# Kernel tuning notes

Measured on AMD Instinct MI355X. Metric: run time of the kernel, lower is better.

## Reference

```python
import jax, jax.numpy as jnp
import numpy as np

N_USERS = 50000
N_PRODS = 50000
N_NODES = N_USERS + N_PRODS
N_EDGES = 600000
UD, PD, H, O = 64, 100, 128, 16


def _gcn_conv(x, W, b, src, dst, n):
    """PyG GCNConv: linear transform, add self-loops, sym-normalized scatter-add."""
    x = x @ W                                    # [n, H]
    loop = jnp.arange(n, dtype=src.dtype)
    src = jnp.concatenate([src, loop])
    dst = jnp.concatenate([dst, loop])
    deg = jax.ops.segment_sum(jnp.ones_like(dst, dtype=x.dtype), dst, num_segments=n)
    dinv = jnp.where(deg > 0, jax.lax.rsqrt(deg), 0.0)
    norm = dinv[src] * dinv[dst]                 # [E+n]
    msg = x[src] * norm[:, None]                 # gather + scale
    out = jax.ops.segment_sum(msg, dst, num_segments=n)
    return out + b


def setup_inputs() -> dict:
    key = jax.random.key(0)
    ks = jax.random.split(key, 16)
    s = 0.05
    return {
        "user_feats": jax.random.normal(ks[0], (N_USERS, UD), dtype=jnp.float32),
        "prod_feats": jax.random.normal(ks[1], (N_PRODS, PD), dtype=jnp.float32),
        "edge_index": jax.random.randint(ks[2], (2, N_EDGES), 0, N_NODES, dtype=jnp.int64),
        "Wu": jax.random.normal(ks[3], (UD, H), dtype=jnp.float32) * s,
        "bu": jnp.zeros((H,), dtype=jnp.float32),
        "Wp": jax.random.normal(ks[4], (PD, H), dtype=jnp.float32) * s,
        "bp": jnp.zeros((H,), dtype=jnp.float32),
        "W1": jax.random.normal(ks[5], (H, H), dtype=jnp.float32) * s,
        "b1": jnp.zeros((H,), dtype=jnp.float32),
        "W2": jax.random.normal(ks[6], (H, H), dtype=jnp.float32) * s,
        "b2": jnp.zeros((H,), dtype=jnp.float32),
        "W3": jax.random.normal(ks[7], (H, H), dtype=jnp.float32) * s,
        "b3": jnp.zeros((H,), dtype=jnp.float32),
        "Wo": jax.random.normal(ks[8], (H, O), dtype=jnp.float32) * s,
        "bo": jnp.zeros((O,), dtype=jnp.float32),
    }


def reference(user_feats, prod_feats, edge_index, Wu, bu, Wp, bp,
              W1, b1, W2, b2, W3, b3, Wo, bo):
    src, dst = edge_index[0], edge_index[1]
    user_x = user_feats @ Wu + bu
    prod_x = prod_feats @ Wp + bp
    x = jnp.concatenate([user_x, prod_x], axis=0)   # [N_NODES, H]
    x = jax.nn.relu(_gcn_conv(x, W1, b1, src, dst, N_NODES))
    # dropout p=0.6 is identity in eval mode
    x = jax.nn.relu(_gcn_conv(x, W2, b2, src, dst, N_NODES))
    x = jax.nn.relu(_gcn_conv(x, W3, b3, src, dst, N_NODES))
    return x @ Wo + bo                              # [N_NODES, O]
```

## Files before the change

kernel.cpp:

```cpp
#include <hip/hip_runtime.h>
#include <hip/hip_fp16.h>

#define NU 50000
#define NP 50000
#define NN 100000
#define NE 600000
#define H  128
#define O  16

typedef __attribute__((ext_vector_type(8))) _Float16 half8;
typedef __attribute__((ext_vector_type(4))) _Float16 h4v;
typedef __attribute__((ext_vector_type(4))) float f32x4;

__global__ void k_prep(const float* __restrict__ Wu, const float* __restrict__ Wp,
                       const float* __restrict__ W1, const float* __restrict__ W2,
                       const float* __restrict__ W3, const float* __restrict__ Wo,
                       __half* __restrict__ whU, __half* __restrict__ wlU,
                       __half* __restrict__ whP, __half* __restrict__ wlP,
                       __half* __restrict__ wh1, __half* __restrict__ wl1,
                       __half* __restrict__ wh2, __half* __restrict__ wl2,
                       __half* __restrict__ wh3, __half* __restrict__ wl3,
                       __half* __restrict__ whO, __half* __restrict__ wlO,
                       int* __restrict__ cnt, int2* __restrict__ epack) {
    int idx = blockIdx.x * blockDim.x + threadIdx.x;
    if (idx >= 75776) {
        int i = idx - 75776;
        if (i < NN) cnt[i] = 0;
        else if (i < NN + 8) { int2 z; z.x = 0; z.y = 0; epack[NE + (i - NN)] = z; }
        return;
    }
    const float* W; __half *Wh, *Wl; int K, KPAD, NC;
    if      (idx <  8192) {              W = Wu; Wh = whU; Wl = wlU; K =  64; KPAD =  64; NC = 128; }
    else if (idx < 24576) { idx -=  8192; W = Wp; Wh = whP; Wl = wlP; K = 100; KPAD = 128; NC = 128; }
    else if (idx < 40960) { idx -= 24576; W = W1; Wh = wh1; Wl = wl1; K = 128; KPAD = 128; NC = 128; }
    else if (idx < 57344) { idx -= 40960; W = W2; Wh = wh2; Wl = wl2; K = 128; KPAD = 128; NC = 128; }
    else if (idx < 73728) { idx -= 57344; W = W3; Wh = wh3; Wl = wl3; K = 128; KPAD = 128; NC = 128; }
    else                  { idx -= 73728; W = Wo; Wh = whO; Wl = wlO; K = 128; KPAD = 128; NC =  16; }
    int n = idx / KPAD, k = idx - n * KPAD;
    float x = (k < K) ? W[k * NC + n] * 16.0f : 0.0f;
    __half h = __float2half_rn(x);
    __half l = __float2half_rn(x - __half2float(h));
    Wh[idx] = h; Wl[idx] = l;
}

__global__ void k_count(const int* __restrict__ dst, int* __restrict__ cnt,
                        int* __restrict__ rank, int E) {
    int e = blockIdx.x * blockDim.x + threadIdx.x;
    if (e < E) rank[e] = atomicAdd(&cnt[dst[e]], 1);
}

#define SCAN_TPB 256
#define SCAN_VPT 4
#define SCAN_CHUNK (SCAN_TPB * SCAN_VPT)

__global__ void k_scan1(const int* __restrict__ in, int* __restrict__ out,
                        int* __restrict__ bsums, float* __restrict__ dinv, int n) {
    __shared__ int sh[SCAN_TPB];
    int t = threadIdx.x, b = blockIdx.x;
    int base = b * SCAN_CHUNK + t * SCAN_VPT;
    int v[SCAN_VPT]; int s = 0;
#pragma unroll
    for (int i = 0; i < SCAN_VPT; i++) {
        int idx = base + i;
        v[i] = (idx < n) ? in[idx] : 0;
        if (idx < n) dinv[idx] = rsqrtf((float)(v[i] + 1));
        s += v[i];
    }
    sh[t] = s; __syncthreads();
    for (int off = 1; off < SCAN_TPB; off <<= 1) {
        int x = (t >= off) ? sh[t - off] : 0;
        __syncthreads();
        sh[t] += x;
        __syncthreads();
    }
    int run = (t > 0) ? sh[t - 1] : 0;
    if (t == SCAN_TPB - 1) bsums[b] = sh[t];
#pragma unroll
    for (int i = 0; i < SCAN_VPT; i++) {
        int idx = base + i;
        if (idx < n) out[idx] = run;
        run += v[i];
    }
}

__global__ void k_scan2(int* __restrict__ bsums, int nb) {
    __shared__ int sh[128];
    int t = threadIdx.x;
    int v = (t < nb) ? bsums[t] : 0;
    sh[t] = v; __syncthreads();
    for (int off = 1; off < 128; off <<= 1) {
        int x = (t >= off) ? sh[t - off] : 0;
        __syncthreads();
        sh[t] += x;
        __syncthreads();
    }
    if (t < nb) bsums[t] = sh[t] - v;
}

__global__ void k_fill(const int* __restrict__ src, const int* __restrict__ dst,
                       const int* __restrict__ offs, const int* __restrict__ bsums,
                       const int* __restrict__ rank, const float* __restrict__ dinv,
                       int2* __restrict__ epack, int E) {
    int e = blockIdx.x * blockDim.x + threadIdx.x;
    if (e < E) {
        int s = src[e], d = dst[e];
        int p = offs[d] + bsums[d >> 10] + rank[e];
        int2 r;
        r.x = s;
        r.y = __float_as_int(dinv[s] * dinv[d]);
        epack[p] = r;
    }
}

template <typename AT, int K, int KPAD, int NI, int MI, int NOUT, bool BIAS, bool F32OUT>
__device__ __forceinline__
void gemm_body(const AT* __restrict__ X,
               const __half* __restrict__ Wh, const __half* __restrict__ Wl,
               const float* __restrict__ bias, void* __restrict__ Cout,
               int M, int orow0, int vb) {
    constexpr int KS = KPAD / 32;
    constexpr int CSPLIT = NOUT / (16 * MI);
    const int tid  = threadIdx.x;
    const int wid  = tid >> 6, lane = tid & 63;
    const int lm   = lane & 15, q = lane >> 4;
    const int gw   = vb * 4 + wid;
    const int tile = gw / CSPLIT;
    const int c0   = (gw % CSPLIT) * (MI * 16);
    const int NT   = (M + NI * 16 - 1) / (NI * 16);
    if (tile >= NT) return;
    const int n0 = tile * (NI * 16);

    half8 wh[MI][KS], wl[MI][KS];
#pragma unroll
    for (int mi = 0; mi < MI; mi++)
#pragma unroll
        for (int ks = 0; ks < KS; ks++) {
            const size_t b = (size_t)(c0 + mi * 16 + lm) * KPAD + ks * 32 + q * 8;
            wh[mi][ks] = *(const half8*)&Wh[b];
            wl[mi][ks] = *(const half8*)&Wl[b];
        }

    f32x4 acc[NI][MI];
#pragma unroll
    for (int ni = 0; ni < NI; ni++)
#pragma unroll
        for (int mi = 0; mi < MI; mi++) acc[ni][mi] = (f32x4)0.0f;

#pragma unroll
    for (int ni = 0; ni < NI; ni++) {
        const int node = n0 + ni * 16 + lm;
        half8 xf[KS];
        if (node < M) {
            if constexpr (sizeof(AT) == 2) {
#pragma unroll
                for (int ks = 0; ks < KS; ks++)
                    xf[ks] = *(const half8*)((const __half*)X + (size_t)node * KPAD + ks * 32 + q * 8);
            } else {
                const float* xp = (const float*)X + (size_t)node * K;
#pragma unroll
                for (int ks = 0; ks < KS; ks++) {
                    const int kb = ks * 32 + q * 8;
                    if (kb + 8 <= K) {
                        float4 v0 = *(const float4*)(xp + kb);
                        float4 v1 = *(const float4*)(xp + kb + 4);
                        xf[ks][0] = (_Float16)v0.x; xf[ks][1] = (_Float16)v0.y;
                        xf[ks][2] = (_Float16)v0.z; xf[ks][3] = (_Float16)v0.w;
                        xf[ks][4] = (_Float16)v1.x; xf[ks][5] = (_Float16)v1.y;
                        xf[ks][6] = (_Float16)v1.z; xf[ks][7] = (_Float16)v1.w;
                    } else if (kb + 4 <= K) {
                        float4 v0 = *(const float4*)(xp + kb);
                        xf[ks][0] = (_Float16)v0.x; xf[ks][1] = (_Float16)v0.y;
                        xf[ks][2] = (_Float16)v0.z; xf[ks][3] = (_Float16)v0.w;
                        xf[ks][4] = (_Float16)0.0f; xf[ks][5] = (_Float16)0.0f;
                        xf[ks][6] = (_Float16)0.0f; xf[ks][7] = (_Float16)0.0f;
                    } else {
#pragma unroll
                        for (int j = 0; j < 8; j++) xf[ks][j] = (_Float16)0.0f;
                    }
                }
            }
        } else {
#pragma unroll
            for (int ks = 0; ks < KS; ks++)
#pragma unroll
                for (int j = 0; j < 8; j++) xf[ks][j] = (_Float16)0.0f;
        }
#pragma unroll
        for (int ks = 0; ks < KS; ks++)
#pragma unroll
            for (int mi = 0; mi < MI; mi++) {
                acc[ni][mi] = __builtin_amdgcn_mfma_f32_16x16x32_f16(wh[mi][ks], xf[ks], acc[ni][mi], 0, 0, 0);
                acc[ni][mi] = __builtin_amdgcn_mfma_f32_16x16x32_f16(wl[mi][ks], xf[ks], acc[ni][mi], 0, 0, 0);
            }
    }

#pragma unroll
    for (int ni = 0; ni < NI; ni++) {
        const int node = n0 + ni * 16 + lm;
        if (node >= M) continue;
#pragma unroll
        for (int mi = 0; mi < MI; mi++) {
            const int cb = c0 + mi * 16 + q * 4;
            float4 bv = BIAS ? *(const float4*)&bias[cb] : make_float4(0.f, 0.f, 0.f, 0.f);
            float v0 = fmaf(acc[ni][mi][0], 0.0625f, bv.x);
            float v1 = fmaf(acc[ni][mi][1], 0.0625f, bv.y);
            float v2 = fmaf(acc[ni][mi][2], 0.0625f, bv.z);
            float v3 = fmaf(acc[ni][mi][3], 0.0625f, bv.w);
            if constexpr (F32OUT) {
                *(float4*)((float*)Cout + (size_t)(orow0 + node) * NOUT + cb) =
                    make_float4(v0, v1, v2, v3);
            } else {
                __half2 h0 = __floats2half2_rn(v0, v1);
                __half2 h1 = __floats2half2_rn(v2, v3);
                uint2 o; o.x = *(unsigned*)&h0; o.y = *(unsigned*)&h1;
                *(uint2*)((__half*)Cout + (size_t)(orow0 + node) * NOUT + cb) = o;
            }
        }
    }
}

template <typename AT, int K, int KPAD, int NI, int MI, int NOUT, bool BIAS, bool F32OUT>
__launch_bounds__(256)
__global__ void k_gemm_reg(const AT* __restrict__ X,
                           const __half* __restrict__ Wh, const __half* __restrict__ Wl,
                           const float* __restrict__ bias, void* __restrict__ Cout,
                           int M, int orow0) {
    gemm_body<AT, K, KPAD, NI, MI, NOUT, BIAS, F32OUT>(X, Wh, Wl, bias, Cout, M, orow0, blockIdx.x);
}

__launch_bounds__(256)
__global__ void k_gemm_inputs(const float* __restrict__ user, const float* __restrict__ prod,
                              const __half* __restrict__ whU, const __half* __restrict__ wlU,
                              const __half* __restrict__ whP, const __half* __restrict__ wlP,
                              const float* __restrict__ bu, const float* __restrict__ bp,
                              void* __restrict__ xA, int blkU) {
    if ((int)blockIdx.x < blkU)
        gemm_body<float,  64,  64, 2, 4, 128, true, false>(user, whU, wlU, bu, xA, NU, 0, blockIdx.x);
    else
        gemm_body<float, 100, 128, 2, 2, 128, true, false>(prod, whP, wlP, bp, xA, NP, NU, blockIdx.x - blkU);
}

__launch_bounds__(256)
__global__ void k_aggregate(const __half* __restrict__ y, const int* __restrict__ offs,
                            const int* __restrict__ bsums, const int2* __restrict__ epack,
                            const float* __restrict__ dinv, const float* __restrict__ bias,
                            __half* __restrict__ out) {
    const int node = __builtin_amdgcn_readfirstlane(blockIdx.x * 4 + (threadIdx.x >> 6));
    const int l = threadIdx.x & 63;
    const int h = l >> 5, j = l & 31;

    int e0 = offs[node] + bsums[node >> 10];
    int e1 = (node + 1 < NN) ? (offs[node + 1] + bsums[(node + 1) >> 10]) : NE;
    e0 = __builtin_amdgcn_readfirstlane(e0);
    e1 = __builtin_amdgcn_readfirstlane(e1);

    const h4v* y4 = (const h4v*)y;

    const float di2 = dinv[node] * dinv[node];
    h4v sv = y4[(size_t)node * 32 + j];
    float4 bv = *(const float4*)&bias[4 * j];

    f32x4 acc0 = (f32x4)0.f, acc1 = (f32x4)0.f, acc2 = (f32x4)0.f, acc3 = (f32x4)0.f;

    for (int e = e0; e < e1; e += 8) {
        const int eb = e + 4 * h;
        const int2* pe = epack + eb;
        int2 p0 = pe[0];
        int2 p1 = pe[1];
        int2 p2 = pe[2];
        int2 p3 = pe[3];
        float w0 = (eb + 0 < e1) ? __int_as_float(p0.y) : 0.f;
        float w1 = (eb + 1 < e1) ? __int_as_float(p1.y) : 0.f;
        float w2 = (eb + 2 < e1) ? __int_as_float(p2.y) : 0.f;
        float w3 = (eb + 3 < e1) ? __int_as_float(p3.y) : 0.f;
        h4v v0 = y4[(size_t)p0.x * 32 + j];
        h4v v1 = y4[(size_t)p1.x * 32 + j];
        h4v v2 = y4[(size_t)p2.x * 32 + j];
        h4v v3 = y4[(size_t)p3.x * 32 + j];
        acc0[0] = fmaf((float)v0[0], w0, acc0[0]); acc0[1] = fmaf((float)v0[1], w0, acc0[1]);
        acc0[2] = fmaf((float)v0[2], w0, acc0[2]); acc0[3] = fmaf((float)v0[3], w0, acc0[3]);
        acc1[0] = fmaf((float)v1[0], w1, acc1[0]); acc1[1] = fmaf((float)v1[1], w1, acc1[1]);
        acc1[2] = fmaf((float)v1[2], w1, acc1[2]); acc1[3] = fmaf((float)v1[3], w1, acc1[3]);
        acc2[0] = fmaf((float)v2[0], w2, acc2[0]); acc2[1] = fmaf((float)v2[1], w2, acc2[1]);
        acc2[2] = fmaf((float)v2[2], w2, acc2[2]); acc2[3] = fmaf((float)v2[3], w2, acc2[3]);
        acc3[0] = fmaf((float)v3[0], w3, acc3[0]); acc3[1] = fmaf((float)v3[1], w3, acc3[1]);
        acc3[2] = fmaf((float)v3[2], w3, acc3[2]); acc3[3] = fmaf((float)v3[3], w3, acc3[3]);
    }

    f32x4 s = (acc0 + acc1) + (acc2 + acc3);
    float t0 = s[0] + __shfl_xor(s[0], 32, 64);
    float t1 = s[1] + __shfl_xor(s[1], 32, 64);
    float t2 = s[2] + __shfl_xor(s[2], 32, 64);
    float t3 = s[3] + __shfl_xor(s[3], 32, 64);

    float r0 = fmaf((float)sv[0], di2, t0) + bv.x;
    float r1 = fmaf((float)sv[1], di2, t1) + bv.y;
    float r2 = fmaf((float)sv[2], di2, t2) + bv.z;
    float r3 = fmaf((float)sv[3], di2, t3) + bv.w;
    if (l < 32) {
        __half2 ha = __floats2half2_rn(fmaxf(r0, 0.f), fmaxf(r1, 0.f));
        __half2 hb = __floats2half2_rn(fmaxf(r2, 0.f), fmaxf(r3, 0.f));
        uint2 o; o.x = *(unsigned*)&ha; o.y = *(unsigned*)&hb;
        *(uint2*)(out + (size_t)node * H + 4 * j) = o;
    }
}

extern "C" void kernel_launch(void* const* d_in, const int* in_sizes, int n_in,
                              void* d_out, int out_size, void* d_ws, size_t ws_size,
                              hipStream_t stream) {
    const float* user = (const float*)d_in[0];
    const float* prod = (const float*)d_in[1];
    const int*   eidx = (const int*)  d_in[2];
    const int*   edst = eidx + NE;
    const int*   esrc = eidx;
    const float* Wu = (const float*)d_in[3];
    const float* bu = (const float*)d_in[4];
    const float* Wp = (const float*)d_in[5];
    const float* bp = (const float*)d_in[6];
    const float* W1 = (const float*)d_in[7];
    const float* b1 = (const float*)d_in[8];
    const float* W2 = (const float*)d_in[9];
    const float* b2 = (const float*)d_in[10];
    const float* W3 = (const float*)d_in[11];
    const float* b3 = (const float*)d_in[12];
    const float* Wo = (const float*)d_in[13];
    const float* bo = (const float*)d_in[14];
    float* out = (float*)d_out;

    char* ws = (char*)d_ws;
    size_t p = 0;
    auto alloc = [&](size_t bytes) -> void* {
        void* r = ws + p;
        p += (bytes + 255) & ~(size_t)255;
        return r;
    };
    __half* xA   = (__half*)alloc((size_t)NN * H * 2);
    __half* xB   = (__half*)alloc((size_t)NN * H * 2);
    int*   cnt   = (int*)  alloc((size_t)NN * 4);
    int*   rank  = (int*)  alloc((size_t)NE * 4);
    int*   offs  = (int*)  alloc((size_t)(NN + 1) * 4);
    float* dinv  = (float*)alloc((size_t)NN * 4);
    int2*  epack = (int2*) alloc((size_t)(NE + 8) * 8);
    int*   bsums = (int*)  alloc(128 * 4);
    __half* whU = (__half*)alloc(128 * 64 * 2);
    __half* wlU = (__half*)alloc(128 * 64 * 2);
    __half* whP = (__half*)alloc(128 * 128 * 2);
    __half* wlP = (__half*)alloc(128 * 128 * 2);
    __half* wh1 = (__half*)alloc(128 * 128 * 2);
    __half* wl1 = (__half*)alloc(128 * 128 * 2);
    __half* wh2 = (__half*)alloc(128 * 128 * 2);
    __half* wl2 = (__half*)alloc(128 * 128 * 2);
    __half* wh3 = (__half*)alloc(128 * 128 * 2);
    __half* wl3 = (__half*)alloc(128 * 128 * 2);
    __half* whO = (__half*)alloc(16 * 128 * 2);
    __half* wlO = (__half*)alloc(16 * 128 * 2);

    const int NBLK = (NN + SCAN_CHUNK - 1) / SCAN_CHUNK;

    k_prep<<<(75776 + NN + 8 + 255) / 256, 256, 0, stream>>>(
        Wu, Wp, W1, W2, W3, Wo,
        whU, wlU, whP, wlP, wh1, wl1, wh2, wl2, wh3, wl3, whO, wlO, cnt, epack);

    k_count<<<(NE + 255) / 256, 256, 0, stream>>>(edst, cnt, rank, NE);
    k_scan1<<<NBLK, SCAN_TPB, 0, stream>>>(cnt, offs, bsums, dinv, NN);
    k_scan2<<<1, 128, 0, stream>>>(bsums, NBLK);
    k_fill <<<(NE + 255) / 256, 256, 0, stream>>>(esrc, edst, offs, bsums, rank, dinv,
                                                  epack, NE);

    {
        constexpr int blkU = (1563 * 2 + 3) / 4;
        constexpr int blkP = (1563 * 4 + 3) / 4;
        k_gemm_inputs<<<blkU + blkP, 256, 0, stream>>>(
            user, prod, whU, wlU, whP, wlP, bu, bp, xA, blkU);
    }

    const int blkG = (1563 * 2 + 3) / 4;
    const int blkO = (1563 + 3) / 4;

    k_gemm_reg<__half, 128, 128, 4, 4, 128, false, false><<<blkG, 256, 0, stream>>>(xA, wh1, wl1, nullptr, xB, NN, 0);
    k_aggregate<<<NN / 4, 256, 0, stream>>>(xB, offs, bsums, epack, dinv, b1, xA);
    k_gemm_reg<__half, 128, 128, 4, 4, 128, false, false><<<blkG, 256, 0, stream>>>(xA, wh2, wl2, nullptr, xB, NN, 0);
    k_aggregate<<<NN / 4, 256, 0, stream>>>(xB, offs, bsums, epack, dinv, b2, xA);
    k_gemm_reg<__half, 128, 128, 4, 4, 128, false, false><<<blkG, 256, 0, stream>>>(xA, wh3, wl3, nullptr, xB, NN, 0);
    k_aggregate<<<NN / 4, 256, 0, stream>>>(xB, offs, bsums, epack, dinv, b3, xA);

    k_gemm_reg<__half, 128, 128, 4, 1, 16, true, true><<<blkO, 256, 0, stream>>>(xA, whO, wlO, bo, out, NN, 0);
}
```

Baseline: 295.6 us.

## Split aggregation across feature slices with 8 edge slots per half-wave

Reworks the neighbor aggregation kernel so each block handles one of 8 feature slices for 8 nodes, with each half-wave processing one node and spreading 8 edges across lane groups of 4. Partial sums are reduced with cross-lane shuffles instead of multiple accumulators. The grid grows to NN blocks, and each block reads a 16-feature column slice of the gathered rows. The aim is more memory-level parallelism and better use of lanes for low-degree nodes. The cost is extra edge-index reloads across slices, more blocks, and divergence when the paired nodes' degrees differ.

```diff
diff --git a/kernel.cpp b/kernel.cpp
--- a/kernel.cpp
+++ b/kernel.cpp
@@ -245,63 +245,58 @@
                             const int* __restrict__ bsums, const int2* __restrict__ epack,
                             const float* __restrict__ dinv, const float* __restrict__ bias,
                             __half* __restrict__ out) {
-    const int node = __builtin_amdgcn_readfirstlane(blockIdx.x * 4 + (threadIdx.x >> 6));
-    const int l = threadIdx.x & 63;
-    const int h = l >> 5, j = l & 31;
+    const int b   = blockIdx.x;
+    const int s   = b & 7;
+    const int wid = threadIdx.x >> 6;
+    const int l   = threadIdx.x & 63;
+    const int h   = l >> 5, hl = l & 31;
+    const int slot = hl >> 2, cl = hl & 3;
+
+    const int node = ((b >> 3) * 4 + wid) * 2 + h;
 
     int e0 = offs[node] + bsums[node >> 10];
     int e1 = (node + 1 < NN) ? (offs[node + 1] + bsums[(node + 1) >> 10]) : NE;
-    e0 = __builtin_amdgcn_readfirstlane(e0);
-    e1 = __builtin_amdgcn_readfirstlane(e1);
+    const int deg  = e1 - e0;
+    const int odeg = __shfl_xor(deg, 32, 64);
+    const int iters = (max(deg, odeg) + 7) >> 3;
 
     const h4v* y4 = (const h4v*)y;
-
+    const int so4 = s * 4 + cl;
+
+    h4v sv = y4[(size_t)node * 32 + so4];
+    float4 bv = *(const float4*)&bias[s * 16 + cl * 4];
     const float di2 = dinv[node] * dinv[node];
-    h4v sv = y4[(size_t)node * 32 + j];
-    float4 bv = *(const float4*)&bias[4 * j];
-
-    f32x4 acc0 = (f32x4)0.f, acc1 = (f32x4)0.f, acc2 = (f32x4)0.f, acc3 = (f32x4)0.f;
-
-    for (int e = e0; e < e1; e += 8) {
-        const int eb = e + 4 * h;
-        const int2* pe = epack + eb;
-        int2 p0 = pe[0];
-        int2 p1 = pe[1];
-        int2 p2 = pe[2];
-        int2 p3 = pe[3];
-        float w0 = (eb + 0 < e1) ? __int_as_float(p0.y) : 0.f;
-        float w1 = (eb + 1 < e1) ? __int_as_float(p1.y) : 0.f;
-        float w2 = (eb + 2 < e1) ? __int_as_float(p2.y) : 0.f;
-        float w3 = (eb + 3 < e1) ? __int_as_float(p3.y) : 0.f;
-        h4v v0 = y4[(size_t)p0.x * 32 + j];
-        h4v v1 = y4[(size_t)p1.x * 32 + j];
-        h4v v2 = y4[(size_t)p2.x * 32 + j];
-        h4v v3 = y4[(size_t)p3.x * 32 + j];
-        acc0[0] = fmaf((float)v0[0], w0, acc0[0]); acc0[1] = fmaf((float)v0[1], w0, acc0[1]);
-        acc0[2] = fmaf((float)v0[2], w0, acc0[2]); acc0[3] = fmaf((float)v0[3], w0, acc0[3]);
-        acc1[0] = fmaf((float)v1[0], w1, acc1[0]); acc1[1] = fmaf((float)v1[1], w1, acc1[1]);
-        acc1[2] = fmaf((float)v1[2], w1, acc1[2]); acc1[3] = fmaf((float)v1[3], w1, acc1[3]);
-        acc2[0] = fmaf((float)v2[0], w2, acc2[0]); acc2[1] = fmaf((float)v2[1], w2, acc2[1]);
-        acc2[2] = fmaf((float)v2[2], w2, acc2[2]); acc2[3] = fmaf((float)v2[3], w2, acc2[3]);
-        acc3[0] = fmaf((float)v3[0], w3, acc3[0]); acc3[1] = fmaf((float)v3[1], w3, acc3[1]);
-        acc3[2] = fmaf((float)v3[2], w3, acc3[2]); acc3[3] = fmaf((float)v3[3], w3, acc3[3]);
-    }
-
-    f32x4 s = (acc0 + acc1) + (acc2 + acc3);
-    float t0 = s[0] + __shfl_xor(s[0], 32, 64);
-    float t1 = s[1] + __shfl_xor(s[1], 32, 64);
-    float t2 = s[2] + __shfl_xor(s[2], 32, 64);
-    float t3 = s[3] + __shfl_xor(s[3], 32, 64);
-
-    float r0 = fmaf((float)sv[0], di2, t0) + bv.x;
-    float r1 = fmaf((float)sv[1], di2, t1) + bv.y;
-    float r2 = fmaf((float)sv[2], di2, t2) + bv.z;
-    float r3 = fmaf((float)sv[3], di2, t3) + bv.w;
-    if (l < 32) {
+
+    f32x4 acc = (f32x4)0.f;
+    for (int it = 0; it < iters; ++it) {
+        const int idx  = e0 + it * 8 + slot;
+        const int lidx = min(idx, NE + 7);
+        int2 p = epack[lidx];
+        float w = (idx < e1) ? __int_as_float(p.y) : 0.f;
+        h4v v = y4[(size_t)p.x * 32 + so4];
+        acc[0] = fmaf((float)v[0], w, acc[0]);
+        acc[1] = fmaf((float)v[1], w, acc[1]);
+        acc[2] = fmaf((float)v[2], w, acc[2]);
+        acc[3] = fmaf((float)v[3], w, acc[3]);
+    }
+
+#pragma unroll
+    for (int m = 4; m <= 16; m <<= 1) {
+        acc[0] += __shfl_xor(acc[0], m, 64);
+        acc[1] += __shfl_xor(acc[1], m, 64);
+        acc[2] += __shfl_xor(acc[2], m, 64);
+        acc[3] += __shfl_xor(acc[3], m, 64);
+    }
+
+    if (slot == 0) {
+        float r0 = fmaf((float)sv[0], di2, acc[0]) + bv.x;
+        float r1 = fmaf((float)sv[1], di2, acc[1]) + bv.y;
+        float r2 = fmaf((float)sv[2], di2, acc[2]) + bv.z;
+        float r3 = fmaf((float)sv[3], di2, acc[3]) + bv.w;
         __half2 ha = __floats2half2_rn(fmaxf(r0, 0.f), fmaxf(r1, 0.f));
         __half2 hb = __floats2half2_rn(fmaxf(r2, 0.f), fmaxf(r3, 0.f));
         uint2 o; o.x = *(unsigned*)&ha; o.y = *(unsigned*)&hb;
-        *(uint2*)(out + (size_t)node * H + 4 * j) = o;
+        *(uint2*)(out + (size_t)node * H + s * 16 + cl * 4) = o;
     }
 }
 
@@ -377,12 +372,14 @@
     const int blkG = (1563 * 2 + 3) / 4;
     const int blkO = (1563 + 3) / 4;
 
+    const int blkA = NN;
+
     k_gemm_reg<__half, 128, 128, 4, 4, 128, false, false><<<blkG, 256, 0, stream>>>(xA, wh1, wl1, nullptr, xB, NN, 0);
-    k_aggregate<<<NN / 4, 256, 0, stream>>>(xB, offs, bsums, epack, dinv, b1, xA);
+    k_aggregate<<<blkA, 256, 0, stream>>>(xB, offs, bsums, epack, dinv, b1, xA);
     k_gemm_reg<__half, 128, 128, 4, 4, 128, false, false><<<blkG, 256, 0, stream>>>(xA, wh2, wl2, nullptr, xB, NN, 0);
-    k_aggregate<<<NN / 4, 256, 0, stream>>>(xB, offs, bsums, epack, dinv, b2, xA);
+    k_aggregate<<<blkA, 256, 0, stream>>>(xB, offs, bsums, epack, dinv, b2, xA);
     k_gemm_reg<__half, 128, 128, 4, 4, 128, false, false><<<blkG, 256, 0, stream>>>(xA, wh3, wl3, nullptr, xB, NN, 0);
-    k_aggregate<<<NN / 4, 256, 0, stream>>>(xB, offs, bsums, epack, dinv, b3, xA);
+    k_aggregate<<<blkA, 256, 0, stream>>>(xB, offs, bsums, epack, dinv, b3, xA);
 
     k_gemm_reg<__half, 128, 128, 4, 1, 16, true, true><<<blkO, 256, 0, stream>>>(xA, whO, wlO, bo, out, NN, 0);
 }
```

New measurement: 550.4 us. 1.86x slower.
